# Optimization experiments

Measured on AMD Instinct MI355X. Metric: run time of the kernel, lower is better.

Reference implementation:

```python
import jax, jax.numpy as jnp
import numpy as np
import math

D = 2048  # hidden_size
B, S = 4, 2048
EPS = 1e-5


def _ln(z, g, b):
    m = jnp.mean(z, axis=-1, keepdims=True)
    v = jnp.mean(jnp.square(z - m), axis=-1, keepdims=True)
    return (z - m) * jax.lax.rsqrt(v + EPS) * g + b


def _rotate_half(x):
    h = x.shape[-1] // 2
    return jnp.concatenate([-x[..., h:], x[..., :h]], axis=-1)


def _mas_normalize(logits):
    m = jnp.max(jnp.abs(logits), axis=-1, keepdims=True)
    return logits / (m + 1e-9)


def setup_inputs() -> dict:
    key = jax.random.key(0)
    ks = jax.random.split(key, 12)
    std = 0.02
    return {
        "x": jax.random.normal(ks[0], (B, S, D), dtype=jnp.float32),
        "position_ids": jnp.arange(S, dtype=jnp.int32),
        "ln1_g": jnp.ones((D,), jnp.float32),
        "ln1_b": jnp.zeros((D,), jnp.float32),
        # stacked params for [q, k, v, o]
        "mu_w": std * jax.random.normal(ks[1], (4, D, D), dtype=jnp.float32),
        "mu_b": jnp.zeros((4, D), jnp.float32),
        "proto_w": std * jax.random.normal(ks[2], (4, D, D), dtype=jnp.float32),
        "gate": jnp.zeros((4, D), jnp.float32),
        "pt_w": std * jax.random.normal(ks[3], (4, D, D), dtype=jnp.float32),
        "pln_g": jnp.ones((4, D), jnp.float32),
        "pln_b": jnp.zeros((4, D), jnp.float32),
        "incoming": std * jax.random.normal(ks[4], (4, D, D), dtype=jnp.float32),
    }


def reference(x, position_ids, ln1_g, ln1_b, mu_w, mu_b, proto_w, gate,
              pt_w, pln_g, pln_b, incoming):
    d = x.shape[-1]
    inv_sqrt_d = 1.0 / math.sqrt(d)

    # proto_state = proto_weight + LN(Linear(incoming))  per module [4, D, D]
    prc = jnp.einsum('nij,noj->nio', incoming, pt_w)
    proto_state = proto_w + _ln(prc, pln_g[:, None, :], pln_b[:, None, :])

    ln1_out = _ln(x, ln1_g, ln1_b)            # [B,S,D]
    ctx = jnp.mean(ln1_out, axis=1)           # [B,D]

    # qkv computation outputs: silu(ln1_out @ mu_w.T + mu_b) for n in {q,k,v}
    comp = jax.nn.silu(jnp.einsum('bsd,nod->nbso', ln1_out, mu_w[:3])
                       + mu_b[:3][:, None, None, :])            # [3,B,S,D]
    # routing from context vector
    match_ctx = jnp.einsum('bd,nod->nbo', ctx, proto_state[:3]) * inv_sqrt_d
    routing = match_ctx + gate[:3][:, None, :]                  # [3,B,D]
    gating = _mas_normalize(routing)
    masked = gating[:, :, None, :] * comp                       # [3,B,S,D]
    q, k, v = masked[0], masked[1], masked[2]

    # RoPE over full hidden dim (num_heads == 1)
    seq = position_ids.shape[0]
    inv_freq = 1.0 / (10000.0 ** (jnp.arange(0, d, 2, dtype=jnp.float32) / d))
    t = jnp.arange(seq, dtype=jnp.float32)
    freqs = t[:, None] * inv_freq[None, :]
    emb = jnp.concatenate([freqs, freqs], axis=-1)              # [S,D]
    cos = jnp.cos(emb)[position_ids]
    sin = jnp.sin(emb)[position_ids]
    q = q * cos + _rotate_half(q) * sin
    k = k * cos + _rotate_half(k) * sin

    # causal single-head attention, scale 1/sqrt(head_dim=D)
    scores = jnp.einsum('bqd,bkd->bqk', q, k) * inv_sqrt_d      # [B,S,S]
    causal = jnp.tril(jnp.ones((seq, seq), dtype=bool))
    scores = jnp.where(causal, scores, jnp.finfo(scores.dtype).min)
    probs = jax.nn.softmax(scores, axis=-1)
    attn_out = jnp.einsum('bqk,bkd->bqd', probs, v)             # [B,S,D]

    # output SPL + routing
    ctx_o = jnp.mean(attn_out, axis=1)
    c_o = jax.nn.silu(jnp.einsum('bsd,od->bso', attn_out, mu_w[3]) + mu_b[3])
    match_o = jnp.einsum('bd,od->bo', ctx_o, proto_state[3]) * inv_sqrt_d
    gating_o = _mas_normalize(match_o + gate[3])
    x_out = x + gating_o[:, None, :] * c_o
    return x_out
```

## Files before the change

### kernel.cpp

```cpp
#include <hip/hip_runtime.h>
#include <hip/hip_bf16.h>
#include <hip/hip_fp16.h>

#define Dh 2048
#define Bh 4
#define Sh 2048
#define NROW 8192
#define HALF 1024
#define INV_SQRT_D 0.022097086912079608f
#define LNEPS 1e-5f

typedef __hip_bfloat16 bf16;
typedef short short8 __attribute__((ext_vector_type(8)));
typedef float f32x4 __attribute__((ext_vector_type(4)));
typedef unsigned short ushort8v __attribute__((ext_vector_type(8)));
typedef unsigned short ushort4v __attribute__((ext_vector_type(4)));

__device__ inline float h2f_bits(unsigned short u) {
  __half h;
  *(unsigned short*)&h = u;
  return __half2float(h);
}
__device__ inline unsigned short bf_bits(float f) {
  bf16 t = __float2bfloat16(f);
  return *(unsigned short*)&t;
}

__device__ inline float warp_sum(float x) {
#pragma unroll
  for (int o = 32; o > 0; o >>= 1) x += __shfl_down(x, o);
  return x;
}
__device__ inline float warp_max(float x) {
#pragma unroll
  for (int o = 32; o > 0; o >>= 1) x = fmaxf(x, __shfl_down(x, o));
  return x;
}
__device__ inline float block_sum(float x, float* sm4) {
  x = warp_sum(x);
  int w = threadIdx.x >> 6;
  if ((threadIdx.x & 63) == 0) sm4[w] = x;
  __syncthreads();
  float r = sm4[0] + sm4[1] + sm4[2] + sm4[3];
  __syncthreads();
  return r;
}
__device__ inline float block_max(float x, float* sm4) {
  x = warp_max(x);
  int w = threadIdx.x >> 6;
  if ((threadIdx.x & 63) == 0) sm4[w] = x;
  __syncthreads();
  float r = fmaxf(fmaxf(sm4[0], sm4[1]), fmaxf(sm4[2], sm4[3]));
  __syncthreads();
  return r;
}

__device__ inline void gload_lds16(const void* g, void* lds) {
  __builtin_amdgcn_global_load_lds(
      (const __attribute__((address_space(1))) unsigned int*)(unsigned long long)g,
      (__attribute__((address_space(3))) unsigned int*)(unsigned long long)lds,
      16, 0, 0);
}

#define MM4(R, AF, B0, B1, B2, B3)                                             \
  acc[R][0] = __builtin_amdgcn_mfma_f32_16x16x32_bf16(AF, B0, acc[R][0], 0, 0, 0); \
  acc[R][1] = __builtin_amdgcn_mfma_f32_16x16x32_bf16(AF, B1, acc[R][1], 0, 0, 0); \
  acc[R][2] = __builtin_amdgcn_mfma_f32_16x16x32_bf16(AF, B2, acc[R][2], 0, 0, 0); \
  acc[R][3] = __builtin_amdgcn_mfma_f32_16x16x32_bf16(AF, B3, acc[R][3], 0, 0, 0);

template <int MODE>
__global__ __launch_bounds__(512) void pgemm(
    const bf16* __restrict__ Aall, const bf16* __restrict__ Ball,
    void* __restrict__ Call, int N, int K, int lda, int ldb,
    long sAz, long sBz, long sCz,
    const float* __restrict__ e0, const float* __restrict__ e1,
    const float* __restrict__ e2, bf16* __restrict__ vt) {
  const int bm0 = blockIdx.x * 256;
  const int bn0 = blockIdx.y * 256;
  if (MODE == 2 && bn0 > bm0 + 255) return;
  const int z = blockIdx.z;
  const bf16* A = Aall + (long)z * sAz;
  const bf16* B = Ball + (long)z * sBz;

  __shared__ __align__(16) char smem[163840];
  const int tid = threadIdx.x;
  const int l = tid & 63, w = tid >> 6;
  const int wr = w >> 2, wc = w & 3;

  f32x4 acc[8][4] = {};
  const int nt = K >> 6;

  const int sg = (((l & 7) ^ ((l >> 3) & 7)) << 3);
  const int srow = (w << 3) + (l >> 3);
  const bf16* aS0 = A + (long)(bm0 + srow) * lda + sg;
  const bf16* aS1 = A + (long)(bm0 + 64 + srow) * lda + sg;
  const bf16* aS2 = A + (long)(bm0 + 128 + srow) * lda + sg;
  const bf16* aS3 = A + (long)(bm0 + 192 + srow) * lda + sg;
  const bf16* bT0 = B + (long)(bn0 + srow) * ldb + sg;
  const bf16* bT1 = B + (long)(bn0 + 64 + srow) * ldb + sg;
  const bf16* bT2 = B + (long)(bn0 + 128 + srow) * ldb + sg;
  const bf16* bT3 = B + (long)(bn0 + 192 + srow) * ldb + sg;
  char* const dA = smem + (w << 10);
  char* const dB = smem + 65536 + (w << 10);

  auto stageA = [&](int tt) {
    int boff = (tt & 1) << 15;
    gload_lds16(aS0 + (tt << 6), dA + boff);
    gload_lds16(aS1 + (tt << 6), dA + boff + 8192);
    gload_lds16(aS2 + (tt << 6), dA + boff + 16384);
    gload_lds16(aS3 + (tt << 6), dA + boff + 24576);
  };
  auto stageB = [&](int tt) {
    int boff = (tt % 3) << 15;
    gload_lds16(bT0 + (tt << 6), dB + boff);
    gload_lds16(bT1 + (tt << 6), dB + boff + 8192);
    gload_lds16(bT2 + (tt << 6), dB + boff + 16384);
    gload_lds16(bT3 + (tt << 6), dB + boff + 24576);
  };

  stageA(0); stageB(0);
  if (nt > 1) stageB(1);
  if (nt > 1) asm volatile("s_waitcnt vmcnt(4)" ::: "memory");
  else        asm volatile("s_waitcnt vmcnt(0)" ::: "memory");
  __builtin_amdgcn_sched_barrier(0);
  asm volatile("s_barrier" ::: "memory");

  const int rslot = (((l >> 4) ^ (l & 7)) << 4);
  const int abyte = (((wr << 7) + (l & 15)) << 7) + rslot;
  const int bbyte = (((wc << 6) + (l & 15)) << 7) + rslot;

  for (int t = 0; t < nt; ++t) {
    const char* Ab = smem + ((t & 1) << 15);
    const char* Bb = smem + 65536 + ((t % 3) << 15);
    short8 b00 = *(const short8*)(Bb + bbyte);
    short8 b01 = *(const short8*)(Bb + bbyte + 2048);
    short8 b02 = *(const short8*)(Bb + bbyte + 4096);
    short8 b03 = *(const short8*)(Bb + bbyte + 6144);
    short8 b10 = *(const short8*)(Bb + (bbyte ^ 64));
    short8 b11 = *(const short8*)(Bb + ((bbyte + 2048) ^ 64));
    short8 b12 = *(const short8*)(Bb + ((bbyte + 4096) ^ 64));
    short8 b13 = *(const short8*)(Bb + ((bbyte + 6144) ^ 64));
    short8 a0 = *(const short8*)(Ab + abyte);
    short8 a1 = *(const short8*)(Ab + abyte + 2048);
    short8 a2 = *(const short8*)(Ab + abyte + 4096);
    short8 a3 = *(const short8*)(Ab + abyte + 6144);
    short8 a4 = *(const short8*)(Ab + abyte + 8192);
    short8 a5 = *(const short8*)(Ab + abyte + 10240);
    short8 a6 = *(const short8*)(Ab + abyte + 12288);
    short8 a7 = *(const short8*)(Ab + abyte + 14336);
    if (t + 1 < nt) stageA(t + 1);
    MM4(0, a0, b00, b01, b02, b03) MM4(1, a1, b00, b01, b02, b03)
    MM4(2, a2, b00, b01, b02, b03) MM4(3, a3, b00, b01, b02, b03)
    MM4(4, a4, b00, b01, b02, b03) MM4(5, a5, b00, b01, b02, b03)
    MM4(6, a6, b00, b01, b02, b03) MM4(7, a7, b00, b01, b02, b03)
    short8 c0 = *(const short8*)(Ab + (abyte ^ 64));
    short8 c1 = *(const short8*)(Ab + ((abyte + 2048) ^ 64));
    short8 c2 = *(const short8*)(Ab + ((abyte + 4096) ^ 64));
    short8 c3 = *(const short8*)(Ab + ((abyte + 6144) ^ 64));
    short8 c4 = *(const short8*)(Ab + ((abyte + 8192) ^ 64));
    short8 c5 = *(const short8*)(Ab + ((abyte + 10240) ^ 64));
    short8 c6 = *(const short8*)(Ab + ((abyte + 12288) ^ 64));
    short8 c7 = *(const short8*)(Ab + ((abyte + 14336) ^ 64));
    if (t + 2 < nt) stageB(t + 2);
    MM4(0, c0, b10, b11, b12, b13) MM4(1, c1, b10, b11, b12, b13)
    MM4(2, c2, b10, b11, b12, b13) MM4(3, c3, b10, b11, b12, b13)
    MM4(4, c4, b10, b11, b12, b13) MM4(5, c5, b10, b11, b12, b13)
    MM4(6, c6, b10, b11, b12, b13) MM4(7, c7, b10, b11, b12, b13)
    if (t < nt - 1) {
      asm volatile("s_waitcnt lgkmcnt(0)" ::: "memory");
      if (t + 2 < nt) asm volatile("s_waitcnt vmcnt(4)" ::: "memory");
      else            asm volatile("s_waitcnt vmcnt(0)" ::: "memory");
      __builtin_amdgcn_sched_barrier(0);
      asm volatile("s_barrier" ::: "memory");
    }
  }

  const int lc = l & 15, lr4 = (l >> 4) << 2;
  if (MODE == 1 && z == 2) {
    unsigned short* tl = (unsigned short*)smem;
    const int bb = bm0 >> 11, s0r = bm0 & 2047;
    __syncthreads();
#pragma unroll
    for (int fr = 0; fr < 8; ++fr) {
      int row0 = (wr << 7) + fr * 16 + lr4;
#pragma unroll
      for (int fc = 0; fc < 4; ++fc) {
        int col = (wc << 6) + fc * 16 + lc;
        int gc = bn0 + col;
        ushort4v u;
#pragma unroll
        for (int qv = 0; qv < 4; ++qv) {
          float val = acc[fr][fc][qv] + e0[2 * Dh + gc];
          float sil = val / (1.f + __expf(-val));
          u[qv] = bf_bits(sil * e1[(2 * Bh + bb) * Dh + gc]);
        }
        *(ushort4v*)(tl + col * 264 + row0) = u;
      }
    }
    __syncthreads();
#pragma unroll
    for (int it = 0; it < 4; ++it) {
      int idx = tid + it * 512;
      int col = idx >> 3, ch = idx & 7;
      const ushort8v* src = (const ushort8v*)(tl + col * 264 + ch * 32);
      ushort8v v0 = src[0], v1 = src[1], v2 = src[2], v3 = src[3];
      ushort8v* dst = (ushort8v*)((unsigned short*)vt +
          ((long)bb * Dh + bn0 + col) * Sh + s0r + ch * 32);
      dst[0] = v0; dst[1] = v1; dst[2] = v2; dst[3] = v3;
    }
  } else {
#pragma unroll
    for (int fr = 0; fr < 8; ++fr) {
      int gr0 = bm0 + (wr << 7) + fr * 16 + lr4;
#pragma unroll
      for (int fc = 0; fc < 4; ++fc) {
        int gc = bn0 + (wc << 6) + fc * 16 + lc;
#pragma unroll
        for (int qv = 0; qv < 4; ++qv) {
          int gr = gr0 + qv;
          float a = acc[fr][fc][qv];
          if (MODE == 0) {
            ((bf16*)Call + (long)z * sCz)[(long)gr * N + gc] =
                __float2bfloat16(a);
          } else if (MODE == 1) {
            float val = a + e0[z * Dh + gc];
            float sil = val / (1.f + __expf(-val));
            int bb = gr >> 11;
            float g = e1[(z * Bh + bb) * Dh + gc];
            ((bf16*)Call + (long)z * sCz)[(long)gr * N + gc] =
                __float2bfloat16(sil * g);
          } else if (MODE == 2) {
            ((__half*)Call + (long)z * sCz)[(long)gr * N + gc] =
                __float2half(a * INV_SQRT_D);
          } else {
            float val = a + e0[gc];
            float sil = val / (1.f + __expf(-val));
            int bb = gr >> 11;
            ((float*)Call)[(long)gr * N + gc] =
                e2[(long)gr * N + gc] + e1[bb * Dh + gc] * sil;
          }
        }
      }
    }
  }
}

__global__ __launch_bounds__(512) void pgemm_h(
    const bf16* __restrict__ Aall, const bf16* __restrict__ Ball,
    bf16* __restrict__ Call, int N, int lda, int ldb,
    long sAz, long sBz, long sCz) {
  const int fid = blockIdx.x;
  const int p = fid >> 8, q = fid & 255;
  const int mh = q >> 5;
  const int z = (q >> 3) & 3, ni = q & 7;
  const int mi = p ? (15 - mh) : mh;
  const int bm0 = mi * 128, bn0 = ni * 256;
  const bf16* A = Aall + (long)z * sAz;
  const bf16* B = Ball + (long)z * sBz;

  __shared__ __align__(16) char smem[131072];
  const int tid = threadIdx.x;
  const int l = tid & 63, w = tid >> 6;
  const int wr = w >> 2, wc = w & 3;
  f32x4 acc[4][4] = {};
  const int nt = (bm0 + 128) >> 6;

  const int sg = (((l & 7) ^ ((l >> 3) & 7)) << 3);
  const int srow = (w << 3) + (l >> 3);
  const bf16* aS0 = A + (long)(bm0 + srow) * lda + sg;
  const bf16* aS1 = A + (long)(bm0 + 64 + srow) * lda + sg;
  const bf16* bT0 = B + (long)(bn0 + srow) * ldb + sg;
  const bf16* bT1 = B + (long)(bn0 + 64 + srow) * ldb + sg;
  const bf16* bT2 = B + (long)(bn0 + 128 + srow) * ldb + sg;
  const bf16* bT3 = B + (long)(bn0 + 192 + srow) * ldb + sg;
  char* const dA = smem + (w << 10);
  char* const dB = smem + 32768 + (w << 10);

  auto stageA = [&](int tt) {
    int boff = (tt & 1) << 14;
    gload_lds16(aS0 + (tt << 6), dA + boff);
    gload_lds16(aS1 + (tt << 6), dA + boff + 8192);
  };
  auto stageB = [&](int tt) {
    int boff = (tt % 3) << 15;
    gload_lds16(bT0 + (tt << 6), dB + boff);
    gload_lds16(bT1 + (tt << 6), dB + boff + 8192);
    gload_lds16(bT2 + (tt << 6), dB + boff + 16384);
    gload_lds16(bT3 + (tt << 6), dB + boff + 24576);
  };

  stageA(0); stageB(0); stageB(1);
  asm volatile("s_waitcnt vmcnt(4)" ::: "memory");
  __builtin_amdgcn_sched_barrier(0);
  asm volatile("s_barrier" ::: "memory");

  const int rslot = (((l >> 4) ^ (l & 7)) << 4);
  const int abyte = (((wr << 6) + (l & 15)) << 7) + rslot;
  const int bbyte = (((wc << 6) + (l & 15)) << 7) + rslot;

  for (int t = 0; t < nt; ++t) {
    const char* Ab = smem + ((t & 1) << 14);
    const char* Bb = smem + 32768 + ((t % 3) << 15);
    short8 b00 = *(const short8*)(Bb + bbyte);
    short8 b01 = *(const short8*)(Bb + bbyte + 2048);
    short8 b02 = *(const short8*)(Bb + bbyte + 4096);
    short8 b03 = *(const short8*)(Bb + bbyte + 6144);
    short8 b10 = *(const short8*)(Bb + (bbyte ^ 64));
    short8 b11 = *(const short8*)(Bb + ((bbyte + 2048) ^ 64));
    short8 b12 = *(const short8*)(Bb + ((bbyte + 4096) ^ 64));
    short8 b13 = *(const short8*)(Bb + ((bbyte + 6144) ^ 64));
    short8 a0 = *(const short8*)(Ab + abyte);
    short8 a1 = *(const short8*)(Ab + abyte + 2048);
    short8 a2 = *(const short8*)(Ab + abyte + 4096);
    short8 a3 = *(const short8*)(Ab + abyte + 6144);
    if (t + 1 < nt) stageA(t + 1);
    MM4(0, a0, b00, b01, b02, b03) MM4(1, a1, b00, b01, b02, b03)
    MM4(2, a2, b00, b01, b02, b03) MM4(3, a3, b00, b01, b02, b03)
    short8 c0 = *(const short8*)(Ab + (abyte ^ 64));
    short8 c1 = *(const short8*)(Ab + ((abyte + 2048) ^ 64));
    short8 c2 = *(const short8*)(Ab + ((abyte + 4096) ^ 64));
    short8 c3 = *(const short8*)(Ab + ((abyte + 6144) ^ 64));
    if (t + 2 < nt) stageB(t + 2);
    MM4(0, c0, b10, b11, b12, b13) MM4(1, c1, b10, b11, b12, b13)
    MM4(2, c2, b10, b11, b12, b13) MM4(3, c3, b10, b11, b12, b13)
    if (t < nt - 1) {
      asm volatile("s_waitcnt lgkmcnt(0)" ::: "memory");
      if (t + 2 < nt) asm volatile("s_waitcnt vmcnt(4)" ::: "memory");
      else            asm volatile("s_waitcnt vmcnt(0)" ::: "memory");
      __builtin_amdgcn_sched_barrier(0);
      asm volatile("s_barrier" ::: "memory");
    }
  }

  const int lc = l & 15, lr4 = (l >> 4) << 2;
  bf16* C = Call + (long)z * sCz;
#pragma unroll
  for (int fr = 0; fr < 4; ++fr) {
    int gr0 = bm0 + (wr << 6) + fr * 16 + lr4;
#pragma unroll
    for (int fc = 0; fc < 4; ++fc) {
      int gc = bn0 + (wc << 6) + fc * 16 + lc;
#pragma unroll
      for (int qv = 0; qv < 4; ++qv)
        C[(long)(gr0 + qv) * N + gc] = __float2bfloat16(acc[fr][fc][qv]);
    }
  }
}

__global__ __launch_bounds__(256) void cvt3_kernel(
    const float* __restrict__ s0, const float* __restrict__ s1,
    const float* __restrict__ s2, bf16* __restrict__ o0, bf16* __restrict__ o1,
    bf16* __restrict__ o2, long n) {
  const float* in = (blockIdx.y == 0) ? s0 : (blockIdx.y == 1) ? s1 : s2;
  bf16* out = (blockIdx.y == 0) ? o0 : (blockIdx.y == 1) ? o1 : o2;
  long i = ((long)blockIdx.x * 256 + threadIdx.x) * 4;
  if (i >= n) return;
  float4 v = *(const float4*)(in + i);
  out[i + 0] = __float2bfloat16(v.x);
  out[i + 1] = __float2bfloat16(v.y);
  out[i + 2] = __float2bfloat16(v.z);
  out[i + 3] = __float2bfloat16(v.w);
}

__global__ __launch_bounds__(256) void ln1_kernel(const float* __restrict__ x,
    const float* __restrict__ g, const float* __restrict__ b, bf16* __restrict__ out) {
  __shared__ float sm4[4];
  long r = blockIdx.x;
  const float* row = x + r * Dh;
  int i0 = threadIdx.x * 4, i1 = 1024 + threadIdx.x * 4;
  float4 v0 = *(const float4*)(row + i0);
  float4 v1 = *(const float4*)(row + i1);
  float s = v0.x + v0.y + v0.z + v0.w + v1.x + v1.y + v1.z + v1.w;
  float s2 = v0.x * v0.x + v0.y * v0.y + v0.z * v0.z + v0.w * v0.w +
             v1.x * v1.x + v1.y * v1.y + v1.z * v1.z + v1.w * v1.w;
  s = block_sum(s, sm4);
  s2 = block_sum(s2, sm4);
  float mean = s * (1.f / Dh);
  float rstd = rsqrtf(s2 * (1.f / Dh) - mean * mean + LNEPS);
  float4 g0 = *(const float4*)(g + i0);
  float4 g1 = *(const float4*)(g + i1);
  float4 b0 = *(const float4*)(b + i0);
  float4 b1 = *(const float4*)(b + i1);
  ushort4v u0, u1;
  u0[0] = bf_bits((v0.x - mean) * rstd * g0.x + b0.x);
  u0[1] = bf_bits((v0.y - mean) * rstd * g0.y + b0.y);
  u0[2] = bf_bits((v0.z - mean) * rstd * g0.z + b0.z);
  u0[3] = bf_bits((v0.w - mean) * rstd * g0.w + b0.w);
  u1[0] = bf_bits((v1.x - mean) * rstd * g1.x + b1.x);
  u1[1] = bf_bits((v1.y - mean) * rstd * g1.y + b1.y);
  u1[2] = bf_bits((v1.z - mean) * rstd * g1.z + b1.z);
  u1[3] = bf_bits((v1.w - mean) * rstd * g1.w + b1.w);
  *(ushort4v*)(out + r * Dh + i0) = u0;
  *(ushort4v*)(out + r * Dh + i1) = u1;
}

__global__ __launch_bounds__(256) void meanrow_kernel(const bf16* __restrict__ in,
                                                      float* __restrict__ outbd) {
  int gid = blockIdx.x * 256 + threadIdx.x;
  int s0 = blockIdx.y * 128;
  long base = ((long)(gid >> 11) * Sh + s0) * Dh + (gid & 2047);
  float s = 0.f;
  for (int t = 0; t < 128; ++t) s += __bfloat162float(in[base + (long)t * Dh]);
  atomicAdd(&outbd[gid], s * (1.f / Sh));
}

__global__ __launch_bounds__(256) void route_kernel(
    const bf16* __restrict__ prc, const float* __restrict__ proto_w,
    const float* __restrict__ pln_g, const float* __restrict__ pln_b,
    const float* __restrict__ gate, const float* __restrict__ ctx,
    float* __restrict__ routing, float* __restrict__ ps3) {
  __shared__ float sm4[4];
  int i = blockIdx.x, n = blockIdx.y;
  long rb = ((long)n * Dh + i) * Dh;
  float v[8];
  float s = 0.f, s2 = 0.f;
#pragma unroll
  for (int c = 0; c < 8; ++c) {
    float t = __bfloat162float(prc[rb + threadIdx.x + c * 256]);
    v[c] = t; s += t; s2 += t * t;
  }
  s = block_sum(s, sm4);
  s2 = block_sum(s2, sm4);
  float mean = s * (1.f / Dh);
  float rstd = rsqrtf(s2 * (1.f / Dh) - mean * mean + LNEPS);
  if (n == 3) {
#pragma unroll
    for (int c = 0; c < 8; ++c) {
      int o = threadIdx.x + c * 256;
      float ps = proto_w[rb + o] + (v[c] - mean) * rstd * pln_g[3 * Dh + o] + pln_b[3 * Dh + o];
      ps3[(long)i * Dh + o] = ps;
    }
  } else {
    float acc[4] = {0.f, 0.f, 0.f, 0.f};
#pragma unroll
    for (int c = 0; c < 8; ++c) {
      int o = threadIdx.x + c * 256;
      float ps = proto_w[rb + o] + (v[c] - mean) * rstd * pln_g[n * Dh + o] + pln_b[n * Dh + o];
#pragma unroll
      for (int b = 0; b < 4; ++b) acc[b] += ps * ctx[b * Dh + o];
    }
    for (int b = 0; b < 4; ++b) {
      float r = block_sum(acc[b], sm4);
      if (threadIdx.x == 0)
        routing[(n * 4 + b) * Dh + i] = r * INV_SQRT_D + gate[n * Dh + i];
    }
  }
}

__global__ __launch_bounds__(256) void route_o_kernel(
    const float* __restrict__ ps3, const float* __restrict__ ctxo,
    const float* __restrict__ gate, float* __restrict__ routing) {
  __shared__ float sm4[4];
  int i = blockIdx.x;
  float acc[4] = {0.f, 0.f, 0.f, 0.f};
#pragma unroll
  for (int c = 0; c < 8; ++c) {
    int o = threadIdx.x + c * 256;
    float p = ps3[(long)i * Dh + o];
#pragma unroll
    for (int b = 0; b < 4; ++b) acc[b] += p * ctxo[b * Dh + o];
  }
  for (int b = 0; b < 4; ++b) {
    float r = block_sum(acc[b], sm4);
    if (threadIdx.x == 0)
      routing[(12 + b) * Dh + i] = r * INV_SQRT_D + gate[3 * Dh + i];
  }
}

__global__ __launch_bounds__(256) void masnorm_kernel(const float* __restrict__ rin,
                                                      float* __restrict__ gout) {
  __shared__ float sm4[4];
  long r = blockIdx.x;
  float m = 0.f;
#pragma unroll
  for (int c = 0; c < 8; ++c)
    m = fmaxf(m, fabsf(rin[r * Dh + threadIdx.x + c * 256]));
  m = block_max(m, sm4);
  float inv = 1.f / (m + 1e-9f);
#pragma unroll
  for (int c = 0; c < 8; ++c) {
    int o = threadIdx.x + c * 256;
    gout[r * Dh + o] = rin[r * Dh + o] * inv;
  }
}

__global__ __launch_bounds__(256) void rope_table_kernel(float* __restrict__ cosT,
                                                         float* __restrict__ sinT) {
  int idx = blockIdx.x * 256 + threadIdx.x;
  int t = idx >> 10, f = idx & 1023;
  float inv_freq = expf(-(float)f * (9.210340371976184f / 1024.f));
  float ang = (float)t * inv_freq;
  cosT[idx] = cosf(ang);
  sinT[idx] = sinf(ang);
}

__global__ __launch_bounds__(256) void rope_kernel(bf16* __restrict__ q, bf16* __restrict__ k,
    const int* __restrict__ pos, const float* __restrict__ cosT,
    const float* __restrict__ sinT) {
  long r = blockIdx.x;
  int s = (int)(r & (Sh - 1));
  int p = pos[s];
#pragma unroll
  for (int c = 0; c < 4; ++c) {
    int t = threadIdx.x + c * 256;
    float cv = cosT[(long)p * HALF + t];
    float sv = sinT[(long)p * HALF + t];
    long i1 = r * Dh + t, i2 = i1 + HALF;
    float q1 = __bfloat162float(q[i1]), q2 = __bfloat162float(q[i2]);
    q[i1] = __float2bfloat16(q1 * cv - q2 * sv);
    q[i2] = __float2bfloat16(q2 * cv + q1 * sv);
    float k1 = __bfloat162float(k[i1]), k2 = __bfloat162float(k[i2]);
    k[i1] = __float2bfloat16(k1 * cv - k2 * sv);
    k[i2] = __float2bfloat16(k2 * cv + k1 * sv);
  }
}

__global__ __launch_bounds__(256) void softmax_kernel(const unsigned short* __restrict__ scores,
                                                      bf16* __restrict__ probs) {
  __shared__ float buf[Sh];
  __shared__ float sm4[4];
  long r = blockIdx.x;
  int qi = (int)(r & (Sh - 1));
  const unsigned short* row = scores + r * (long)Sh;
  bf16* prow = probs + r * (long)Sh;
  int tid = threadIdx.x;
  int n = qi + 1, nv = n & ~7;
  float m = -3.0e38f;
  for (int o = tid * 8; o < nv; o += 2048) {
    ushort8v v = *(const ushort8v*)(row + o);
#pragma unroll
    for (int j = 0; j < 8; ++j) {
      float x = h2f_bits(v[j]);
      buf[o + j] = x;
      m = fmaxf(m, x);
    }
  }
  for (int o = nv + tid; o < n; o += 256) {
    float x = h2f_bits(row[o]); buf[o] = x; m = fmaxf(m, x);
  }
  m = block_max(m, sm4);
  float s = 0.f;
  for (int o = tid; o < n; o += 256) {
    float e = __expf(buf[o] - m); buf[o] = e; s += e;
  }
  s = block_sum(s, sm4);
  float inv = 1.f / s;
  for (int o = tid * 8; o < nv; o += 2048) {
    ushort8v u;
#pragma unroll
    for (int j = 0; j < 8; ++j) u[j] = bf_bits(buf[o + j] * inv);
    *(ushort8v*)(prow + o) = u;
  }
  for (int o = nv + tid; o < n; o += 256) prow[o] = __float2bfloat16(buf[o] * inv);
  int zlim = (qi & ~127) + 128;
  int za = (n + 7) & ~7;
  for (int o = n + tid; o < za && o < zlim; o += 256) prow[o] = __float2bfloat16(0.f);
  ushort8v zz = {0, 0, 0, 0, 0, 0, 0, 0};
  for (int o = za + tid * 8; o < zlim; o += 2048) *(ushort8v*)(prow + o) = zz;
}

extern "C" void kernel_launch(void* const* d_in, const int* in_sizes, int n_in,
                              void* d_out, int out_size, void* d_ws, size_t ws_size,
                              hipStream_t stream) {
  const float* x       = (const float*)d_in[0];
  const int*   pos     = (const int*)d_in[1];
  const float* ln1_g   = (const float*)d_in[2];
  const float* ln1_b   = (const float*)d_in[3];
  const float* mu_w    = (const float*)d_in[4];
  const float* mu_b    = (const float*)d_in[5];
  const float* proto_w = (const float*)d_in[6];
  const float* gate    = (const float*)d_in[7];
  const float* pt_w    = (const float*)d_in[8];
  const float* pln_g   = (const float*)d_in[9];
  const float* pln_b   = (const float*)d_in[10];
  const float* incoming= (const float*)d_in[11];

  char* w = (char*)d_ws;
  const long BF = 33554432L;
  bf16*  ln1    = (bf16*)(w);
  bf16*  qb     = (bf16*)(w + BF);
  bf16*  kb     = (bf16*)(w + 2 * BF);
  bf16*  vb     = (bf16*)(w + 3 * BF);
  bf16*  attn   = (bf16*)(w + 4 * BF);
  bf16*  mu_wb  = (bf16*)(w + 5 * BF);
  bf16*  ptw_b  = (bf16*)(w + 6 * BF);
  bf16*  vT     = ptw_b;
  bf16*  inc_b  = (bf16*)(w + 7 * BF);
  bf16*  probs  = inc_b;
  float* ps3    = (float*)(w + 8 * BF);
  float* cosT   = (float*)(w + 8 * BF + 16777216L);
  float* sinT   = cosT + (long)Sh * HALF;
  float* ctx    = sinT + (long)Sh * HALF;
  float* ctxo   = ctx + Bh * Dh;
  float* routing= ctxo + Bh * Dh;
  float* gating = routing + 16 * Dh;
  bf16*   prc    = (bf16*)d_out;
  __half* scores = (__half*)d_out;
  (void)vb;

  const long DD4 = 4L * Dh * Dh;

  hipMemsetAsync(ctx, 0, 2L * Bh * Dh * sizeof(float), stream);

  rope_table_kernel<<<(Sh * HALF) / 256, 256, 0, stream>>>(cosT, sinT);
  cvt3_kernel<<<dim3(DD4 / 1024, 3), 256, 0, stream>>>(
      mu_w, incoming, pt_w, mu_wb, inc_b, ptw_b, DD4);
  ln1_kernel<<<NROW, 256, 0, stream>>>(x, ln1_g, ln1_b, ln1);
  meanrow_kernel<<<dim3(32, 16), 256, 0, stream>>>(ln1, ctx);
  pgemm<0><<<dim3(8, 8, 4), 512, 0, stream>>>(
      inc_b, ptw_b, prc, Dh, Dh, Dh, Dh,
      (long)Dh * Dh, (long)Dh * Dh, (long)Dh * Dh,
      nullptr, nullptr, nullptr, nullptr);
  route_kernel<<<dim3(Dh, 4), 256, 0, stream>>>(prc, proto_w, pln_g, pln_b,
                                                gate, ctx, routing, ps3);
  masnorm_kernel<<<12, 256, 0, stream>>>(routing, gating);
  pgemm<1><<<dim3(32, 8, 3), 512, 0, stream>>>(
      ln1, mu_wb, qb, Dh, Dh, Dh, Dh,
      0L, (long)Dh * Dh, (long)NROW * Dh, mu_b, gating, nullptr, vT);
  rope_kernel<<<NROW, 256, 0, stream>>>(qb, kb, pos, cosT, sinT);
  pgemm<2><<<dim3(8, 8, 4), 512, 0, stream>>>(
      qb, kb, scores, Sh, Dh, Dh, Dh,
      (long)Sh * Dh, (long)Sh * Dh, (long)Sh * Sh,
      nullptr, nullptr, nullptr, nullptr);
  softmax_kernel<<<Bh * Sh, 256, 0, stream>>>((const unsigned short*)scores, probs);
  pgemm_h<<<512, 512, 0, stream>>>(
      probs, vT, attn, Dh, Sh, Sh,
      (long)Sh * Sh, (long)Dh * Sh, (long)Sh * Dh);
  meanrow_kernel<<<dim3(32, 16), 256, 0, stream>>>(attn, ctxo);
  route_o_kernel<<<Dh, 256, 0, stream>>>(ps3, ctxo, gate, routing);
  masnorm_kernel<<<4, 256, 0, stream>>>(routing + 12 * Dh, gating + 12 * Dh);
  pgemm<4><<<dim3(32, 8, 1), 512, 0, stream>>>(
      attn, mu_wb + 3L * Dh * Dh, d_out, Dh, Dh, Dh, Dh,
      0L, 0L, 0L, mu_b + 3 * Dh, gating + 12 * Dh, x, nullptr);
}
```

Before: 602.0 us.

## Restructure GEMM main loop into four barrier-separated quadrant phases with setprio

The main K-loop of the bf16 MFMA GEMM is split into four phases. Each phase loads a subset of A/B fragments from LDS, issues part of the global-to-LDS prefetch, then runs 16 MFMAs at raised wave priority (s_setprio), with s_barrier between phases. The aim is to interleave global loads, LDS reads and MFMA work across waves in a ping-pong style and to cut register pressure from holding all 16 A fragments at once. In exchange it adds several block-wide barriers per iteration and fragments are reloaded (a/c reused across halves), which could stall waves if the phases are unbalanced.

```diff
diff --git a/kernel.cpp b/kernel.cpp
--- a/kernel.cpp
+++ b/kernel.cpp
@@ -61,6 +61,9 @@
       (__attribute__((address_space(3))) unsigned int*)(unsigned long long)lds,
       16, 0, 0);
 }
+
+#define MMQ(FR, FC, AV, BV)                                                    \
+  acc[FR][FC] = __builtin_amdgcn_mfma_f32_16x16x32_bf16(AV, BV, acc[FR][FC], 0, 0, 0);
 
 #define MM4(R, AF, B0, B1, B2, B3)                                             \
   acc[R][0] = __builtin_amdgcn_mfma_f32_16x16x32_bf16(AF, B0, acc[R][0], 0, 0, 0); \
@@ -132,42 +135,93 @@
   for (int t = 0; t < nt; ++t) {
     const char* Ab = smem + ((t & 1) << 15);
     const char* Bb = smem + 65536 + ((t % 3) << 15);
+    short8 a0, a1, a2, a3, c0, c1, c2, c3;
+
     short8 b00 = *(const short8*)(Bb + bbyte);
     short8 b01 = *(const short8*)(Bb + bbyte + 2048);
+    short8 b10 = *(const short8*)(Bb + (bbyte ^ 64));
+    short8 b11 = *(const short8*)(Bb + ((bbyte + 2048) ^ 64));
+    a0 = *(const short8*)(Ab + abyte);
+    a1 = *(const short8*)(Ab + abyte + 2048);
+    a2 = *(const short8*)(Ab + abyte + 4096);
+    a3 = *(const short8*)(Ab + abyte + 6144);
+    c0 = *(const short8*)(Ab + (abyte ^ 64));
+    c1 = *(const short8*)(Ab + ((abyte + 2048) ^ 64));
+    c2 = *(const short8*)(Ab + ((abyte + 4096) ^ 64));
+    c3 = *(const short8*)(Ab + ((abyte + 6144) ^ 64));
+    if (t + 1 < nt) {
+      int boff = ((t + 1) & 1) << 15;
+      gload_lds16(aS0 + ((t + 1) << 6), dA + boff);
+      gload_lds16(aS1 + ((t + 1) << 6), dA + boff + 8192);
+    }
+    asm volatile("s_barrier" ::: "memory");
+    asm volatile("s_waitcnt lgkmcnt(0)" ::: "memory");
+    __builtin_amdgcn_sched_barrier(0);
+    __builtin_amdgcn_s_setprio(1);
+    MMQ(0, 0, a0, b00) MMQ(1, 0, a1, b00) MMQ(2, 0, a2, b00) MMQ(3, 0, a3, b00)
+    MMQ(0, 1, a0, b01) MMQ(1, 1, a1, b01) MMQ(2, 1, a2, b01) MMQ(3, 1, a3, b01)
+    MMQ(0, 0, c0, b10) MMQ(1, 0, c1, b10) MMQ(2, 0, c2, b10) MMQ(3, 0, c3, b10)
+    MMQ(0, 1, c0, b11) MMQ(1, 1, c1, b11) MMQ(2, 1, c2, b11) MMQ(3, 1, c3, b11)
+    __builtin_amdgcn_s_setprio(0);
+    asm volatile("s_barrier" ::: "memory");
+
     short8 b02 = *(const short8*)(Bb + bbyte + 4096);
     short8 b03 = *(const short8*)(Bb + bbyte + 6144);
-    short8 b10 = *(const short8*)(Bb + (bbyte ^ 64));
-    short8 b11 = *(const short8*)(Bb + ((bbyte + 2048) ^ 64));
     short8 b12 = *(const short8*)(Bb + ((bbyte + 4096) ^ 64));
     short8 b13 = *(const short8*)(Bb + ((bbyte + 6144) ^ 64));
-    short8 a0 = *(const short8*)(Ab + abyte);
-    short8 a1 = *(const short8*)(Ab + abyte + 2048);
-    short8 a2 = *(const short8*)(Ab + abyte + 4096);
-    short8 a3 = *(const short8*)(Ab + abyte + 6144);
-    short8 a4 = *(const short8*)(Ab + abyte + 8192);
-    short8 a5 = *(const short8*)(Ab + abyte + 10240);
-    short8 a6 = *(const short8*)(Ab + abyte + 12288);
-    short8 a7 = *(const short8*)(Ab + abyte + 14336);
-    if (t + 1 < nt) stageA(t + 1);
-    MM4(0, a0, b00, b01, b02, b03) MM4(1, a1, b00, b01, b02, b03)
-    MM4(2, a2, b00, b01, b02, b03) MM4(3, a3, b00, b01, b02, b03)
-    MM4(4, a4, b00, b01, b02, b03) MM4(5, a5, b00, b01, b02, b03)
-    MM4(6, a6, b00, b01, b02, b03) MM4(7, a7, b00, b01, b02, b03)
-    short8 c0 = *(const short8*)(Ab + (abyte ^ 64));
-    short8 c1 = *(const short8*)(Ab + ((abyte + 2048) ^ 64));
-    short8 c2 = *(const short8*)(Ab + ((abyte + 4096) ^ 64));
-    short8 c3 = *(const short8*)(Ab + ((abyte + 6144) ^ 64));
-    short8 c4 = *(const short8*)(Ab + ((abyte + 8192) ^ 64));
-    short8 c5 = *(const short8*)(Ab + ((abyte + 10240) ^ 64));
-    short8 c6 = *(const short8*)(Ab + ((abyte + 12288) ^ 64));
-    short8 c7 = *(const short8*)(Ab + ((abyte + 14336) ^ 64));
-    if (t + 2 < nt) stageB(t + 2);
-    MM4(0, c0, b10, b11, b12, b13) MM4(1, c1, b10, b11, b12, b13)
-    MM4(2, c2, b10, b11, b12, b13) MM4(3, c3, b10, b11, b12, b13)
-    MM4(4, c4, b10, b11, b12, b13) MM4(5, c5, b10, b11, b12, b13)
-    MM4(6, c6, b10, b11, b12, b13) MM4(7, c7, b10, b11, b12, b13)
+    if (t + 1 < nt) {
+      int boff = ((t + 1) & 1) << 15;
+      gload_lds16(aS2 + ((t + 1) << 6), dA + boff + 16384);
+      gload_lds16(aS3 + ((t + 1) << 6), dA + boff + 24576);
+    }
+    asm volatile("s_barrier" ::: "memory");
+    asm volatile("s_waitcnt lgkmcnt(0)" ::: "memory");
+    __builtin_amdgcn_sched_barrier(0);
+    __builtin_amdgcn_s_setprio(1);
+    MMQ(0, 2, a0, b02) MMQ(1, 2, a1, b02) MMQ(2, 2, a2, b02) MMQ(3, 2, a3, b02)
+    MMQ(0, 3, a0, b03) MMQ(1, 3, a1, b03) MMQ(2, 3, a2, b03) MMQ(3, 3, a3, b03)
+    MMQ(0, 2, c0, b12) MMQ(1, 2, c1, b12) MMQ(2, 2, c2, b12) MMQ(3, 2, c3, b12)
+    MMQ(0, 3, c0, b13) MMQ(1, 3, c1, b13) MMQ(2, 3, c2, b13) MMQ(3, 3, c3, b13)
+    __builtin_amdgcn_s_setprio(0);
+    asm volatile("s_barrier" ::: "memory");
+
+    a0 = *(const short8*)(Ab + abyte + 8192);
+    a1 = *(const short8*)(Ab + abyte + 10240);
+    a2 = *(const short8*)(Ab + abyte + 12288);
+    a3 = *(const short8*)(Ab + abyte + 14336);
+    c0 = *(const short8*)(Ab + ((abyte + 8192) ^ 64));
+    c1 = *(const short8*)(Ab + ((abyte + 10240) ^ 64));
+    c2 = *(const short8*)(Ab + ((abyte + 12288) ^ 64));
+    c3 = *(const short8*)(Ab + ((abyte + 14336) ^ 64));
+    if (t + 2 < nt) {
+      int boff = ((t + 2) % 3) << 15;
+      gload_lds16(bT0 + ((t + 2) << 6), dB + boff);
+      gload_lds16(bT1 + ((t + 2) << 6), dB + boff + 8192);
+    }
+    asm volatile("s_barrier" ::: "memory");
+    asm volatile("s_waitcnt lgkmcnt(0)" ::: "memory");
+    __builtin_amdgcn_sched_barrier(0);
+    __builtin_amdgcn_s_setprio(1);
+    MMQ(4, 2, a0, b02) MMQ(5, 2, a1, b02) MMQ(6, 2, a2, b02) MMQ(7, 2, a3, b02)
+    MMQ(4, 3, a0, b03) MMQ(5, 3, a1, b03) MMQ(6, 3, a2, b03) MMQ(7, 3, a3, b03)
+    MMQ(4, 2, c0, b12) MMQ(5, 2, c1, b12) MMQ(6, 2, c2, b12) MMQ(7, 2, c3, b12)
+    MMQ(4, 3, c0, b13) MMQ(5, 3, c1, b13) MMQ(6, 3, c2, b13) MMQ(7, 3, c3, b13)
+    __builtin_amdgcn_s_setprio(0);
+    asm volatile("s_barrier" ::: "memory");
+
+    if (t + 2 < nt) {
+      int boff = ((t + 2) % 3) << 15;
+      gload_lds16(bT2 + ((t + 2) << 6), dB + boff + 16384);
+      gload_lds16(bT3 + ((t + 2) << 6), dB + boff + 24576);
+    }
+    asm volatile("s_barrier" ::: "memory");
+    __builtin_amdgcn_s_setprio(1);
+    MMQ(4, 0, a0, b00) MMQ(5, 0, a1, b00) MMQ(6, 0, a2, b00) MMQ(7, 0, a3, b00)
+    MMQ(4, 1, a0, b01) MMQ(5, 1, a1, b01) MMQ(6, 1, a2, b01) MMQ(7, 1, a3, b01)
+    MMQ(4, 0, c0, b10) MMQ(5, 0, c1, b10) MMQ(6, 0, c2, b10) MMQ(7, 0, c3, b10)
+    MMQ(4, 1, c0, b11) MMQ(5, 1, c1, b11) MMQ(6, 1, c2, b11) MMQ(7, 1, c3, b11)
+    __builtin_amdgcn_s_setprio(0);
     if (t < nt - 1) {
-      asm volatile("s_waitcnt lgkmcnt(0)" ::: "memory");
       if (t + 2 < nt) asm volatile("s_waitcnt vmcnt(4)" ::: "memory");
       else            asm volatile("s_waitcnt vmcnt(0)" ::: "memory");
       __builtin_amdgcn_sched_barrier(0);
```

Measured after the change: 643.1 us. +6.8%, slower.
